# Kernel tuning notes

Measured on AMD Instinct MI355X. Metric: run time of the kernel, lower is better.

## Reference

```python
import jax, jax.numpy as jnp
import numpy as np

VOCAB = 100000
HIDDEN = 128
BATCH = 1024
LEN = 200


def setup_inputs() -> dict:
    key = jax.random.key(0)
    k_ids, k_w, k_b = jax.random.split(key, 3)
    word_ids = jax.random.randint(k_ids, (BATCH, LEN), 0, VOCAB)
    # nn.Linear(vocab_sz, hidden_sz): weight [hidden, vocab], bias [hidden]
    bound = 1.0 / np.sqrt(VOCAB)
    W = jax.random.uniform(k_w, (HIDDEN, VOCAB), jnp.float32, -bound, bound)
    b = jax.random.uniform(k_b, (HIDDEN,), jnp.float32, -bound, bound)
    return {"word_ids": word_ids, "W": W, "b": b}


def reference(word_ids, W, b):
    B, L = word_ids.shape
    # bag-of-words histogram: count occurrences of each word per scene
    rows = jnp.broadcast_to(jnp.arange(B)[:, None], (B, L))  # [B, L]
    hist = jnp.zeros((B, W.shape[1]), dtype=W.dtype).at[rows, word_ids].add(1.0)
    # dense linear: y = hist @ W^T + b
    return jnp.einsum("bv,hv->bh", hist, W) + b
```

## Files before the change

kernel.cpp:

```cpp
#include <hip/hip_runtime.h>
#include <hip/hip_fp16.h>

#define VOCAB 100000
#define HIDDEN 128
#define BATCH 1024
#define LEN 200
#define TP_V 64

typedef float f32x4 __attribute__((ext_vector_type(4)));

__global__ __launch_bounds__(256) void wt_transpose_f16(
    const float* __restrict__ W, __half* __restrict__ WT) {
    __shared__ float tile[TP_V][133];
    const int v0 = blockIdx.x * TP_V;
    const int t  = threadIdx.x;

    const int vx = t & 15;
    const int hy = t >> 4;
#pragma unroll
    for (int p = 0; p < 8; ++p) {
        const int h  = hy + p * 16;
        const int gv = v0 + vx * 4;
        f32x4 f;
        if (gv + 3 < VOCAB) {
            f = __builtin_nontemporal_load(
                reinterpret_cast<const f32x4*>(&W[(size_t)h * VOCAB + gv]));
        } else {
            f[0] = (gv + 0 < VOCAB) ? W[(size_t)h * VOCAB + gv + 0] : 0.f;
            f[1] = (gv + 1 < VOCAB) ? W[(size_t)h * VOCAB + gv + 1] : 0.f;
            f[2] = (gv + 2 < VOCAB) ? W[(size_t)h * VOCAB + gv + 2] : 0.f;
            f[3] = (gv + 3 < VOCAB) ? W[(size_t)h * VOCAB + gv + 3] : 0.f;
        }
        tile[vx * 4 + 0][h] = f[0];
        tile[vx * 4 + 1][h] = f[1];
        tile[vx * 4 + 2][h] = f[2];
        tile[vx * 4 + 3][h] = f[3];
    }
    __syncthreads();

    const int h8 = (t & 15) * 8;
#pragma unroll
    for (int p = 0; p < 4; ++p) {
        const int v  = (t >> 4) + p * 16;
        const int gv = v0 + v;
        if (gv < VOCAB) {
            __half hb[8];
#pragma unroll
            for (int k = 0; k < 8; ++k) hb[k] = __float2half_rn(tile[v][h8 + k]);
            *reinterpret_cast<float4*>(&WT[(size_t)gv * HIDDEN + h8]) =
                *reinterpret_cast<const float4*>(hb);
        }
    }
}

__global__ __launch_bounds__(512) void bag_gather_f16(
    const int* __restrict__ ids, const __half* __restrict__ WT,
    const float* __restrict__ bias, float* __restrict__ out) {
    __shared__ int   sid[LEN];
    __shared__ float part[8][HIDDEN];

    const int b = blockIdx.x;
    const int t = threadIdx.x;

    for (int l = t; l < LEN; l += 512) sid[l] = ids[b * LEN + l];
    __syncthreads();

    const int g     = t & 15;
    const int chunk = t >> 4;

    float acc[8];
#pragma unroll
    for (int k = 0; k < 8; ++k) acc[k] = 0.f;

    for (int l = chunk; l < LEN; l += 32) {
        const int id = sid[l];
        const float4 q = *reinterpret_cast<const float4*>(
            WT + (size_t)id * HIDDEN + g * 8);
        const __half2* h2 = reinterpret_cast<const __half2*>(&q);
#pragma unroll
        for (int k = 0; k < 4; ++k) {
            const float2 f = __half22float2(h2[k]);
            acc[2 * k + 0] += f.x;
            acc[2 * k + 1] += f.y;
        }
    }

#pragma unroll
    for (int k = 0; k < 8; ++k) {
        acc[k] += __shfl_xor(acc[k], 16);
        acc[k] += __shfl_xor(acc[k], 32);
    }
    const int wave = t >> 6;
    if ((t & 63) < 16) {
#pragma unroll
        for (int k = 0; k < 8; ++k) part[wave][g * 8 + k] = acc[k];
    }
    __syncthreads();

    if (t < HIDDEN) {
        float s = 0.f;
#pragma unroll
        for (int w = 0; w < 8; ++w) s += part[w][t];
        out[(size_t)b * HIDDEN + t] = s + bias[t];
    }
}

__global__ __launch_bounds__(HIDDEN) void bag_direct_kernel(
    const int* __restrict__ ids, const float* __restrict__ W,
    const float* __restrict__ bias, float* __restrict__ out) {
    __shared__ int sid[LEN];
    const int b = blockIdx.x;
    const int h = threadIdx.x;
    for (int l = h; l < LEN; l += HIDDEN) sid[l] = ids[b * LEN + l];
    __syncthreads();
    float acc = 0.f;
    for (int l = 0; l < LEN; ++l)
        acc += W[(size_t)h * VOCAB + sid[l]];
    out[(size_t)b * HIDDEN + h] = acc + bias[h];
}

extern "C" void kernel_launch(void* const* d_in, const int* in_sizes, int n_in,
                              void* d_out, int out_size, void* d_ws, size_t ws_size,
                              hipStream_t stream) {
    const int*   ids  = (const int*)d_in[0];
    const float* W    = (const float*)d_in[1];
    const float* bias = (const float*)d_in[2];
    float*       out  = (float*)d_out;

    const size_t need = (size_t)VOCAB * HIDDEN * sizeof(__half);
    if (ws_size >= need) {
        __half* WT = (__half*)d_ws;
        wt_transpose_f16<<<(VOCAB + TP_V - 1) / TP_V, 256, 0, stream>>>(W, WT);
        bag_gather_f16<<<BATCH, 512, 0, stream>>>(ids, WT, bias, out);
    } else {
        bag_direct_kernel<<<BATCH, HIDDEN, 0, stream>>>(ids, W, bias, out);
    }
}
```

Before: 108.9 us.

## Widen transpose tiles with swizzled fp16 LDS and unroll gather loop

The transpose kernel now handles 256 vocab entries per block with 512 threads. It converts to fp16 before writing to shared memory and uses an XOR swizzle in place of padding to avoid bank conflicts, so LDS use halves and each row read is 256 contiguous floats. The gather kernel's loop is fully unrolled to 7 iterations with predicated loads, so more independent loads can be in flight at once. The cost is higher register pressure and a few wasted loads of row 0 for out-of-range slots.

```diff
diff --git a/kernel.cpp b/kernel.cpp
--- a/kernel.cpp
+++ b/kernel.cpp
@@ -5,22 +5,22 @@
 #define HIDDEN 128
 #define BATCH 1024
 #define LEN 200
-#define TP_V 64
+#define TP_V 256
 
 typedef float f32x4 __attribute__((ext_vector_type(4)));
 
-__global__ __launch_bounds__(256) void wt_transpose_f16(
+__global__ __launch_bounds__(512) void wt_transpose_f16(
     const float* __restrict__ W, __half* __restrict__ WT) {
-    __shared__ float tile[TP_V][133];
+    __shared__ __half tile[TP_V][HIDDEN];
     const int v0 = blockIdx.x * TP_V;
     const int t  = threadIdx.x;
 
-    const int vx = t & 15;
-    const int hy = t >> 4;
+    const int vq4 = t & 63;
+    const int hr  = t >> 6;
 #pragma unroll
-    for (int p = 0; p < 8; ++p) {
-        const int h  = hy + p * 16;
-        const int gv = v0 + vx * 4;
+    for (int p = 0; p < 16; ++p) {
+        const int h  = p * 8 + hr;
+        const int gv = v0 + vq4 * 4;
         f32x4 f;
         if (gv + 3 < VOCAB) {
             f = __builtin_nontemporal_load(
@@ -31,23 +31,26 @@
             f[2] = (gv + 2 < VOCAB) ? W[(size_t)h * VOCAB + gv + 2] : 0.f;
             f[3] = (gv + 3 < VOCAB) ? W[(size_t)h * VOCAB + gv + 3] : 0.f;
         }
-        tile[vx * 4 + 0][h] = f[0];
-        tile[vx * 4 + 1][h] = f[1];
-        tile[vx * 4 + 2][h] = f[2];
-        tile[vx * 4 + 3][h] = f[3];
+#pragma unroll
+        for (int k = 0; k < 4; ++k) {
+            const int v = vq4 * 4 + k;
+            tile[v][h ^ ((v & 31) << 1)] = __float2half_rn(f[k]);
+        }
     }
     __syncthreads();
 
-    const int h8 = (t & 15) * 8;
+    const int c  = t & 15;
+    const int vr = t >> 4;
 #pragma unroll
-    for (int p = 0; p < 4; ++p) {
-        const int v  = (t >> 4) + p * 16;
+    for (int q = 0; q < 8; ++q) {
+        const int v  = vr + q * 32;
         const int gv = v0 + v;
         if (gv < VOCAB) {
             __half hb[8];
+            const int sw = (v & 31) << 1;
 #pragma unroll
-            for (int k = 0; k < 8; ++k) hb[k] = __float2half_rn(tile[v][h8 + k]);
-            *reinterpret_cast<float4*>(&WT[(size_t)gv * HIDDEN + h8]) =
+            for (int j = 0; j < 8; ++j) hb[j] = tile[v][(c * 8 + j) ^ sw];
+            *reinterpret_cast<float4*>(&WT[(size_t)gv * HIDDEN + c * 8]) =
                 *reinterpret_cast<const float4*>(hb);
         }
     }
@@ -72,16 +75,21 @@
 #pragma unroll
     for (int k = 0; k < 8; ++k) acc[k] = 0.f;
 
-    for (int l = chunk; l < LEN; l += 32) {
-        const int id = sid[l];
+#pragma unroll
+    for (int i = 0; i < 7; ++i) {
+        const int  l  = chunk + i * 32;
+        const bool ok = (l < LEN);
+        const int  id = ok ? sid[l] : 0;
         const float4 q = *reinterpret_cast<const float4*>(
             WT + (size_t)id * HIDDEN + g * 8);
-        const __half2* h2 = reinterpret_cast<const __half2*>(&q);
+        if (ok) {
+            const __half2* h2 = reinterpret_cast<const __half2*>(&q);
 #pragma unroll
-        for (int k = 0; k < 4; ++k) {
-            const float2 f = __half22float2(h2[k]);
-            acc[2 * k + 0] += f.x;
-            acc[2 * k + 1] += f.y;
+            for (int k = 0; k < 4; ++k) {
+                const float2 f = __half22float2(h2[k]);
+                acc[2 * k + 0] += f.x;
+                acc[2 * k + 1] += f.y;
+            }
         }
     }
 
@@ -130,7 +138,7 @@
     const size_t need = (size_t)VOCAB * HIDDEN * sizeof(__half);
     if (ws_size >= need) {
         __half* WT = (__half*)d_ws;
-        wt_transpose_f16<<<(VOCAB + TP_V - 1) / TP_V, 256, 0, stream>>>(W, WT);
+        wt_transpose_f16<<<(VOCAB + TP_V - 1) / TP_V, 512, 0, stream>>>(W, WT);
         bag_gather_f16<<<BATCH, 512, 0, stream>>>(ids, WT, bias, out);
     } else {
         bag_direct_kernel<<<BATCH, HIDDEN, 0, stream>>>(ids, W, bias, out);
```

Measured after the change: 107.7 us. About the same (-1.1%).
